# Kernel tuning notes

Measured on AMD Instinct MI355X. Metric: run time of the kernel, lower is better.

## Reference

```python
import jax, jax.numpy as jnp
import numpy as np

N = 100000   # nodes
E = 1600000  # edges
G = 512      # graphs in batch
F_IN = 128
H = 128
F_OUT = 1


def setup_inputs() -> dict:
    key = jax.random.key(0)
    ks = jax.random.split(key, 12)
    x = jax.random.normal(ks[0], (N, F_IN), dtype=jnp.float32)
    src = jax.random.randint(ks[1], (E,), 0, N, dtype=jnp.int32)
    dst = jax.random.randint(ks[2], (E,), 0, N, dtype=jnp.int32)
    node2graph = jnp.sort(jax.random.randint(ks[3], (N,), 0, G, dtype=jnp.int32))
    s_in = 1.0 / np.sqrt(F_IN)
    s_h = 1.0 / np.sqrt(H)
    W0 = jax.random.normal(ks[4], (F_IN, H), dtype=jnp.float32) * s_in
    b0 = jnp.zeros((H,), dtype=jnp.float32)
    W1 = jax.random.normal(ks[5], (H, H), dtype=jnp.float32) * s_h
    b1 = jnp.zeros((H,), dtype=jnp.float32)
    W2 = jax.random.normal(ks[6], (H, H), dtype=jnp.float32) * s_h
    b2 = jnp.zeros((H,), dtype=jnp.float32)
    Wm1 = jax.random.normal(ks[7], (H, H), dtype=jnp.float32) * s_h
    bm1 = jnp.zeros((H,), dtype=jnp.float32)
    Wm2 = jax.random.normal(ks[8], (H, F_OUT), dtype=jnp.float32) * s_h
    bm2 = jnp.zeros((F_OUT,), dtype=jnp.float32)
    return {"x": x, "src": src, "dst": dst, "node2graph": node2graph,
            "W0": W0, "b0": b0, "W1": W1, "b1": b1, "W2": W2, "b2": b2,
            "Wm1": Wm1, "bm1": bm1, "Wm2": Wm2, "bm2": bm2}


def _degree_norms(src, dst):
    ones = jnp.ones((E,), dtype=jnp.float32)
    out_deg = jax.ops.segment_sum(ones, src, num_segments=N)
    in_deg = jax.ops.segment_sum(ones, dst, num_segments=N)
    norm_out = jax.lax.rsqrt(jnp.maximum(out_deg, 1.0))  # [N]
    norm_in = jax.lax.rsqrt(jnp.maximum(in_deg, 1.0))    # [N]
    return norm_out, norm_in


def _graph_conv(x, src, dst, norm_out, norm_in, W, b):
    # DGL GraphConv, norm='both', in_feats <= out_feats path:
    # aggregate normalized src features, then linear + activation.
    xs = x * norm_out[:, None]
    msg = xs[src]                                         # [E, H] gather
    agg = jax.ops.segment_sum(msg, dst, num_segments=N)   # [N, H] scatter-add
    agg = agg * norm_in[:, None]
    return jax.nn.relu(agg @ W + b)


def reference(x, src, dst, node2graph, W0, b0, W1, b1, W2, b2, Wm1, bm1, Wm2, bm2):
    norm_out, norm_in = _degree_norms(src, dst)
    h = _graph_conv(x, src, dst, norm_out, norm_in, W0, b0)
    h = _graph_conv(h, src, dst, norm_out, norm_in, W1, b1)
    h = _graph_conv(h, src, dst, norm_out, norm_in, W2, b2)
    # sum_nodes readout per graph
    g = jax.ops.segment_sum(h, node2graph, num_segments=G)  # [G, H]
    # MLP head: Linear -> ReLU -> Linear
    return jax.nn.relu(g @ Wm1 + bm1) @ Wm2 + bm2           # [G, 1]
```

## Files before the change

### kernel.cpp

```cpp
#include <hip/hip_runtime.h>

#define NN 100000
#define NE 1600000
#define NG 512
#define HD 128

#define NBK 196
#define CHUNK 5120
#define NC 313
#define LH (2 * NBK * NC)

typedef _Float16 h8 __attribute__((ext_vector_type(8)));
typedef float f32x4 __attribute__((ext_vector_type(4)));

__global__ __launch_bounds__(1024) void k_hist(const int* __restrict__ src,
                                               const int* __restrict__ dst,
                                               int* __restrict__ H,
                                               const float* __restrict__ W0,
                                               const float* __restrict__ W1,
                                               const float* __restrict__ W2,
                                               _Float16* __restrict__ Bt) {
    if (blockIdx.x >= NC) {
        int i = (blockIdx.x - NC) * 1024 + threadIdx.x;
        int w = i >> 14;
        int rem = i & 16383;
        int n = rem >> 7;
        int k = rem & 127;
        const float* W = (w == 0) ? W0 : ((w == 1) ? W1 : W2);
        Bt[i] = (_Float16)W[k * 128 + n];
        return;
    }
    __shared__ int hd[NBK], hs[NBK];
    int c = blockIdx.x;
    for (int i = threadIdx.x; i < NBK; i += 1024) { hd[i] = 0; hs[i] = 0; }
    __syncthreads();
    int e0 = c * CHUNK;
    int e1 = e0 + CHUNK; if (e1 > NE) e1 = NE;
    for (int e = e0 + threadIdx.x; e < e1; e += 1024) {
        atomicAdd(&hd[dst[e] >> 9], 1);
        atomicAdd(&hs[src[e] >> 9], 1);
    }
    __syncthreads();
    for (int i = threadIdx.x; i < NBK; i += 1024) {
        H[i * NC + c] = hd[i];
        H[NBK * NC + i * NC + c] = hs[i];
    }
}

__global__ __launch_bounds__(256) void k_scan1g(int* __restrict__ H,
                                                int* __restrict__ bsum, int L) {
    __shared__ int s[256];
    int i = blockIdx.x * 256 + threadIdx.x;
    int v = (i < L) ? H[i] : 0;
    s[threadIdx.x] = v;
    __syncthreads();
    for (int off = 1; off < 256; off <<= 1) {
        int t = (threadIdx.x >= off) ? s[threadIdx.x - off] : 0;
        __syncthreads();
        s[threadIdx.x] += t;
        __syncthreads();
    }
    if (i < L) H[i] = s[threadIdx.x] - v;
    if (threadIdx.x == 255) bsum[blockIdx.x] = s[255];
}

__global__ __launch_bounds__(256) void k_scan3g(int* __restrict__ H,
                                                const int* __restrict__ bsum,
                                                int L, int nb) {
    __shared__ int sb[512];
    __shared__ int tmp2[256];
    int t = threadIdx.x;
    int b0 = (2 * t < nb) ? bsum[2 * t] : 0;
    int b1 = (2 * t + 1 < nb) ? bsum[2 * t + 1] : 0;
    int pair = b0 + b1;
    tmp2[t] = pair;
    __syncthreads();
    for (int off = 1; off < 256; off <<= 1) {
        int v2 = (t >= off) ? tmp2[t - off] : 0;
        __syncthreads();
        tmp2[t] += v2;
        __syncthreads();
    }
    int ex = tmp2[t] - pair;
    sb[2 * t] = ex;
    sb[2 * t + 1] = ex + b0;
    __syncthreads();
    int i = blockIdx.x * 256 + t;
    if (i < L) H[i] += sb[i >> 8];
}

__global__ __launch_bounds__(1024) void k_scatter(const int* __restrict__ src,
                                                  const int* __restrict__ dst,
                                                  const int* __restrict__ H,
                                                  int* __restrict__ dpart,
                                                  unsigned short* __restrict__ spart) {
    __shared__ int cd[NBK], cs[NBK];
    int c = blockIdx.x;
    for (int i = threadIdx.x; i < NBK; i += 1024) {
        cd[i] = H[i * NC + c];
        cs[i] = H[NBK * NC + i * NC + c] - NE;
    }
    __syncthreads();
    int e0 = c * CHUNK;
    int e1 = e0 + CHUNK; if (e1 > NE) e1 = NE;
    for (int e = e0 + threadIdx.x; e < e1; e += 1024) {
        int s = src[e], d = dst[e];
        int pd = atomicAdd(&cd[d >> 9], 1);
        dpart[pd] = s | ((d & 511) << 17);
        int ps = atomicAdd(&cs[s >> 9], 1);
        spart[ps] = (unsigned short)(s & 511);
    }
}

__global__ __launch_bounds__(1024) void k_bucket(const int* __restrict__ dpart,
                                                 const unsigned short* __restrict__ spart,
                                                 const int* __restrict__ H,
                                                 int* __restrict__ offs,
                                                 int* __restrict__ csr,
                                                 float* __restrict__ ni,
                                                 float* __restrict__ no) {
    __shared__ int deg[512];
    __shared__ int cur[512];
    __shared__ int tmp[1024];
    int b = blockIdx.x;
    bool isDst = (b < NBK);
    int bb = isDst ? b : b - NBK;
    int start, end;
    if (isDst) {
        start = H[bb * NC];
        end = (bb + 1 < NBK) ? H[(bb + 1) * NC] : NE;
    } else {
        start = H[NBK * NC + bb * NC] - NE;
        end = (bb + 1 < NBK) ? H[NBK * NC + (bb + 1) * NC] - NE : NE;
    }
    int t = threadIdx.x;
    if (t < 512) deg[t] = 0;
    __syncthreads();
    if (isDst) {
        for (int i = start + t; i < end; i += 1024)
            atomicAdd(&deg[(dpart[i] >> 17) & 511], 1);
    } else {
        for (int i = start + t; i < end; i += 1024)
            atomicAdd(&deg[spart[i]], 1);
    }
    __syncthreads();
    int vb = bb * 512;
    if (!isDst) {
        if (t < 512) {
            int v = vb + t;
            if (v < NN) no[v] = rsqrtf(fmaxf((float)deg[t], 1.0f));
        }
        return;
    }
    int a = (t < 512) ? deg[t] : 0;
    tmp[t] = a;
    __syncthreads();
    for (int off = 1; off < 1024; off <<= 1) {
        int v2 = (t >= off) ? tmp[t - off] : 0;
        __syncthreads();
        tmp[t] += v2;
        __syncthreads();
    }
    if (t < 512) {
        cur[t] = start + tmp[t] - a;
        int v = vb + t;
        if (v < NN) {
            offs[v] = cur[t];
            ni[v] = rsqrtf(fmaxf((float)a, 1.0f));
        }
    }
    if (b == NBK - 1 && t == 0) offs[NN] = NE;
    __syncthreads();
    for (int i = start + t; i < end; i += 1024) {
        int pk = dpart[i];
        int p = atomicAdd(&cur[(pk >> 17) & 511], 1);
        csr[p] = pk & 0x1FFFF;
    }
}

template <typename TA>
__global__ __launch_bounds__(256) void k_gemm_mfma(const TA* __restrict__ A,
                                                   const _Float16* __restrict__ Bt,
                                                   const float* __restrict__ no,
                                                   _Float16* __restrict__ Zh,
                                                   int nrows) {
    __shared__ _Float16 Bs[128 * 136];
    int tid = threadIdx.x;
    {
        const h8* B8 = (const h8*)Bt;
        h8* Bs8 = (h8*)Bs;
        for (int i = tid; i < 2048; i += 256) {
            int n = i >> 4, c = i & 15;
            Bs8[n * 17 + c] = B8[i];
        }
    }

    int wave = tid >> 6;
    int lane = tid & 63;
    int m16 = lane & 15;
    int quad = lane >> 4;
    int rowbase = blockIdx.x * 64 + wave * 16;
    int row = rowbase + m16;
    bool valid = row < nrows;

    h8 afrag[4];
    if (valid) {
        if constexpr (sizeof(TA) == 2) {
            const h8* Arow = (const h8*)(A + (size_t)row * 128);
#pragma unroll
            for (int kk = 0; kk < 4; kk++) afrag[kk] = Arow[kk * 4 + quad];
        } else {
            const float4* Arow = (const float4*)(A + (size_t)row * 128);
#pragma unroll
            for (int kk = 0; kk < 4; kk++) {
                float4 lo = Arow[kk * 8 + quad * 2];
                float4 hi = Arow[kk * 8 + quad * 2 + 1];
                h8 a;
                a[0] = (_Float16)lo.x; a[1] = (_Float16)lo.y;
                a[2] = (_Float16)lo.z; a[3] = (_Float16)lo.w;
                a[4] = (_Float16)hi.x; a[5] = (_Float16)hi.y;
                a[6] = (_Float16)hi.z; a[7] = (_Float16)hi.w;
                afrag[kk] = a;
            }
        }
    } else {
#pragma unroll
        for (int kk = 0; kk < 4; kk++) {
            h8 a;
#pragma unroll
            for (int j = 0; j < 8; j++) a[j] = (_Float16)0.f;
            afrag[kk] = a;
        }
    }

    __syncthreads();

    f32x4 acc[8];
#pragma unroll
    for (int nt = 0; nt < 8; nt++) acc[nt] = (f32x4){0.f, 0.f, 0.f, 0.f};

    const h8* Bs8 = (const h8*)Bs;
#pragma unroll
    for (int nt = 0; nt < 8; nt++) {
        const h8* Bp = Bs8 + (size_t)(nt * 16 + m16) * 17;
#pragma unroll
        for (int kk = 0; kk < 4; kk++) {
            acc[nt] = __builtin_amdgcn_mfma_f32_16x16x32_f16(afrag[kk], Bp[kk * 4 + quad],
                                                             acc[nt], 0, 0, 0);
        }
    }

    float nor[4];
#pragma unroll
    for (int r = 0; r < 4; r++) {
        int grow = rowbase + quad * 4 + r;
        nor[r] = (grow < nrows) ? no[grow] : 0.f;
    }

    __syncthreads();
    {
        int lr0 = wave * 16 + quad * 4;
#pragma unroll
        for (int nt = 0; nt < 8; nt++) {
#pragma unroll
            for (int r = 0; r < 4; r++) {
                Bs[(size_t)(lr0 + r) * 136 + nt * 16 + m16] =
                    (_Float16)(acc[nt][r] * nor[r]);
            }
        }
    }
    __syncthreads();

    int blockrow0 = blockIdx.x * 64;
    for (int i = tid; i < 1024; i += 256) {
        int r = i >> 4, cch = i & 15;
        int grow = blockrow0 + r;
        if (grow < nrows) {
            h8 val = *(const h8*)&Bs[(size_t)r * 136 + cch * 8];
            *(h8*)&Zh[(size_t)grow * 128 + cch * 8] = val;
        }
    }
}

__global__ __launch_bounds__(256) void k_agg(const h8* __restrict__ Zh,
                                             const int* __restrict__ offs,
                                             const int* __restrict__ csr,
                                             const float* __restrict__ ni,
                                             const float* __restrict__ b,
                                             h8* __restrict__ H16) {
    int v = blockIdx.x * 16 + (threadIdx.x >> 4);
    int c = threadIdx.x & 15;
    int s = offs[v];
    int e = offs[v + 1];
    float a0[8], a1[8];
#pragma unroll
    for (int j = 0; j < 8; j++) { a0[j] = 0.f; a1[j] = 0.f; }
    int i = s;
    for (; i + 4 <= e; i += 4) {
        int u0 = csr[i];
        int u1 = csr[i + 1];
        int u2 = csr[i + 2];
        int u3 = csr[i + 3];
        h8 z0 = Zh[(size_t)u0 * 16 + c];
        h8 z1 = Zh[(size_t)u1 * 16 + c];
        h8 z2 = Zh[(size_t)u2 * 16 + c];
        h8 z3 = Zh[(size_t)u3 * 16 + c];
#pragma unroll
        for (int j = 0; j < 8; j++) {
            a0[j] += (float)z0[j] + (float)z1[j];
            a1[j] += (float)z2[j] + (float)z3[j];
        }
    }
    for (; i < e; i++) {
        int u = csr[i];
        h8 z = Zh[(size_t)u * 16 + c];
#pragma unroll
        for (int j = 0; j < 8; j++) a0[j] += (float)z[j];
    }
    float niv = ni[v];
    const float* bb = b + c * 8;
    h8 r;
#pragma unroll
    for (int j = 0; j < 8; j++)
        r[j] = (_Float16)fmaxf((a0[j] + a1[j]) * niv + bb[j], 0.f);
    H16[(size_t)v * 16 + c] = r;
}

__global__ __launch_bounds__(256) void k_gsum(const h8* __restrict__ H8,
                                              const int* __restrict__ n2g,
                                              float* __restrict__ gbuf) {
    __shared__ float red[256 * 8];
    int gi = blockIdx.x >> 2;
    int part = blockIdx.x & 3;
    int t = threadIdx.x;
    int slot = t >> 4;
    int c = t & 15;

    int lo = 0, hi = NN;
    while (lo < hi) { int mid = (lo + hi) >> 1; if (n2g[mid] < gi) lo = mid + 1; else hi = mid; }
    int s = lo;
    hi = NN;
    while (lo < hi) { int mid = (lo + hi) >> 1; if (n2g[mid] < gi + 1) lo = mid + 1; else hi = mid; }
    int e = lo;

    float acc[8];
#pragma unroll
    for (int j = 0; j < 8; j++) acc[j] = 0.f;
    for (int v = s + part * 16 + slot; v < e; v += 64) {
        h8 z = H8[(size_t)v * 16 + c];
#pragma unroll
        for (int j = 0; j < 8; j++) acc[j] += (float)z[j];
    }
#pragma unroll
    for (int j = 0; j < 8; j++) red[t * 8 + j] = acc[j];
    __syncthreads();
    for (int off = 8; off >= 1; off >>= 1) {
        if (slot < off) {
#pragma unroll
            for (int j = 0; j < 8; j++)
                red[t * 8 + j] += red[(t + off * 16) * 8 + j];
        }
        __syncthreads();
    }
    if (slot == 0) {
#pragma unroll
        for (int j = 0; j < 8; j++)
            gbuf[((size_t)part * NG + gi) * 128 + c * 8 + j] = red[t * 8 + j];
    }
}

__global__ __launch_bounds__(128) void k_head(const float* __restrict__ gbuf,
                                              const float* __restrict__ Wm1,
                                              const float* __restrict__ bm1,
                                              const float* __restrict__ Wm2,
                                              const float* __restrict__ bm2,
                                              float* __restrict__ out) {
    __shared__ float gs[128];
    __shared__ float red2[128];
    int gi = blockIdx.x;
    int t = threadIdx.x;
    gs[t] = gbuf[(size_t)gi * 128 + t] +
            gbuf[((size_t)NG + gi) * 128 + t] +
            gbuf[((size_t)2 * NG + gi) * 128 + t] +
            gbuf[((size_t)3 * NG + gi) * 128 + t];
    __syncthreads();
    float a = bm1[t];
    for (int k = 0; k < 128; k++) a += gs[k] * Wm1[k * 128 + t];
    red2[t] = fmaxf(a, 0.f) * Wm2[t];
    __syncthreads();
    for (int s2 = 64; s2 > 0; s2 >>= 1) {
        if (t < s2) red2[t] += red2[t + s2];
        __syncthreads();
    }
    if (t == 0) out[gi] = red2[0] + bm2[0];
}

extern "C" void kernel_launch(void* const* d_in, const int* in_sizes, int n_in,
                              void* d_out, int out_size, void* d_ws, size_t ws_size,
                              hipStream_t stream) {
    const float* x   = (const float*)d_in[0];
    const int*   src = (const int*)d_in[1];
    const int*   dst = (const int*)d_in[2];
    const int*   n2g = (const int*)d_in[3];
    const float* W0  = (const float*)d_in[4];
    const float* b0  = (const float*)d_in[5];
    const float* W1  = (const float*)d_in[6];
    const float* b1  = (const float*)d_in[7];
    const float* W2  = (const float*)d_in[8];
    const float* b2  = (const float*)d_in[9];
    const float* Wm1 = (const float*)d_in[10];
    const float* bm1 = (const float*)d_in[11];
    const float* Wm2 = (const float*)d_in[12];
    const float* bm2 = (const float*)d_in[13];
    float* out = (float*)d_out;

    char* p = (char*)d_ws;
    auto carve = [&](size_t bytes) -> char* {
        char* r = p;
        p += (bytes + 255) & ~(size_t)255;
        return r;
    };
    _Float16* zh  = (_Float16*)carve((size_t)NN * HD * 2);
    _Float16* h16 = (_Float16*)carve((size_t)NN * HD * 2);
    _Float16* Bt  = (_Float16*)carve((size_t)3 * 128 * 128 * 2);
    float* no     = (float*)carve((size_t)NN * 4);
    float* ni     = (float*)carve((size_t)NN * 4);
    int*   offs   = (int*)carve((size_t)(NN + 1) * 4);
    int*   csr    = (int*)carve((size_t)NE * 4);
    int*   Hh     = (int*)carve((size_t)LH * 4);
    int*   bsum   = (int*)carve((size_t)512 * 4);
    int*   dpart  = (int*)carve((size_t)NE * 4);
    unsigned short* spart = (unsigned short*)carve((size_t)NE * 2);
    float* gbuf   = (float*)carve((size_t)4 * NG * 128 * 4);

    int scan_blocks = (LH + 255) / 256;
    k_hist<<<NC + 48, 1024, 0, stream>>>(src, dst, Hh, W0, W1, W2, Bt);
    k_scan1g<<<scan_blocks, 256, 0, stream>>>(Hh, bsum, LH);
    k_scan3g<<<scan_blocks, 256, 0, stream>>>(Hh, bsum, LH, scan_blocks);
    k_scatter<<<NC, 1024, 0, stream>>>(src, dst, Hh, dpart, spart);
    k_bucket<<<2 * NBK, 1024, 0, stream>>>(dpart, spart, Hh, offs, csr, ni, no);

    int gemm_blocks = (NN + 63) / 64;
    int agg_blocks  = NN / 16;

    k_gemm_mfma<float><<<gemm_blocks, 256, 0, stream>>>(x, Bt, no, zh, NN);
    k_agg<<<agg_blocks, 256, 0, stream>>>((const h8*)zh, offs, csr, ni, b0, (h8*)h16);
    k_gemm_mfma<_Float16><<<gemm_blocks, 256, 0, stream>>>(h16, Bt + 16384, no, zh, NN);
    k_agg<<<agg_blocks, 256, 0, stream>>>((const h8*)zh, offs, csr, ni, b1, (h8*)h16);
    k_gemm_mfma<_Float16><<<gemm_blocks, 256, 0, stream>>>(h16, Bt + 32768, no, zh, NN);
    k_agg<<<agg_blocks, 256, 0, stream>>>((const h8*)zh, offs, csr, ni, b2, (h8*)h16);

    k_gsum<<<NG * 4, 256, 0, stream>>>((const h8*)h16, n2g, gbuf);
    k_head<<<NG, 128, 0, stream>>>(gbuf, Wm1, bm1, Wm2, bm2, out);
}
```

Baseline: 387.0 us.

## Replace per-chunk histogram scan with global bucket totals and atomic cursor allocation

The edge partitioning no longer keeps a per-chunk histogram with a two-pass global scan. It now accumulates global bucket totals with atomics, scans only 392 entries in a single block, and has each scatter block reserve its output ranges with atomics on a global cursor. This drops one scan kernel and the large histogram buffer, and the chunk size is halved. In exchange, each scatter block recounts its edges, and the order of edges within a bucket becomes nondeterministic, which can change float summation order downstream.

```diff
diff --git a/kernel.cpp b/kernel.cpp
--- a/kernel.cpp
+++ b/kernel.cpp
@@ -6,22 +6,22 @@
 #define HD 128
 
 #define NBK 196
-#define CHUNK 5120
-#define NC 313
-#define LH (2 * NBK * NC)
+#define NB2 392
+#define CHUNK2 2560
+#define NC2 625
 
 typedef _Float16 h8 __attribute__((ext_vector_type(8)));
 typedef float f32x4 __attribute__((ext_vector_type(4)));
 
-__global__ __launch_bounds__(1024) void k_hist(const int* __restrict__ src,
-                                               const int* __restrict__ dst,
-                                               int* __restrict__ H,
-                                               const float* __restrict__ W0,
-                                               const float* __restrict__ W1,
-                                               const float* __restrict__ W2,
-                                               _Float16* __restrict__ Bt) {
-    if (blockIdx.x >= NC) {
-        int i = (blockIdx.x - NC) * 1024 + threadIdx.x;
+__global__ __launch_bounds__(1024) void k_count(const int* __restrict__ src,
+                                                const int* __restrict__ dst,
+                                                int* __restrict__ Btot,
+                                                const float* __restrict__ W0,
+                                                const float* __restrict__ W1,
+                                                const float* __restrict__ W2,
+                                                _Float16* __restrict__ Bt) {
+    if (blockIdx.x >= NC2) {
+        int i = (blockIdx.x - NC2) * 1024 + threadIdx.x;
         int w = i >> 14;
         int rem = i & 16383;
         int n = rem >> 7;
@@ -30,91 +30,72 @@
         Bt[i] = (_Float16)W[k * 128 + n];
         return;
     }
-    __shared__ int hd[NBK], hs[NBK];
-    int c = blockIdx.x;
-    for (int i = threadIdx.x; i < NBK; i += 1024) { hd[i] = 0; hs[i] = 0; }
-    __syncthreads();
-    int e0 = c * CHUNK;
-    int e1 = e0 + CHUNK; if (e1 > NE) e1 = NE;
-    for (int e = e0 + threadIdx.x; e < e1; e += 1024) {
-        atomicAdd(&hd[dst[e] >> 9], 1);
-        atomicAdd(&hs[src[e] >> 9], 1);
-    }
-    __syncthreads();
-    for (int i = threadIdx.x; i < NBK; i += 1024) {
-        H[i * NC + c] = hd[i];
-        H[NBK * NC + i * NC + c] = hs[i];
-    }
-}
-
-__global__ __launch_bounds__(256) void k_scan1g(int* __restrict__ H,
-                                                int* __restrict__ bsum, int L) {
-    __shared__ int s[256];
-    int i = blockIdx.x * 256 + threadIdx.x;
-    int v = (i < L) ? H[i] : 0;
-    s[threadIdx.x] = v;
-    __syncthreads();
-    for (int off = 1; off < 256; off <<= 1) {
-        int t = (threadIdx.x >= off) ? s[threadIdx.x - off] : 0;
-        __syncthreads();
-        s[threadIdx.x] += t;
-        __syncthreads();
-    }
-    if (i < L) H[i] = s[threadIdx.x] - v;
-    if (threadIdx.x == 255) bsum[blockIdx.x] = s[255];
-}
-
-__global__ __launch_bounds__(256) void k_scan3g(int* __restrict__ H,
-                                                const int* __restrict__ bsum,
-                                                int L, int nb) {
-    __shared__ int sb[512];
-    __shared__ int tmp2[256];
-    int t = threadIdx.x;
-    int b0 = (2 * t < nb) ? bsum[2 * t] : 0;
-    int b1 = (2 * t + 1 < nb) ? bsum[2 * t + 1] : 0;
-    int pair = b0 + b1;
-    tmp2[t] = pair;
-    __syncthreads();
-    for (int off = 1; off < 256; off <<= 1) {
-        int v2 = (t >= off) ? tmp2[t - off] : 0;
-        __syncthreads();
-        tmp2[t] += v2;
-        __syncthreads();
-    }
-    int ex = tmp2[t] - pair;
-    sb[2 * t] = ex;
-    sb[2 * t + 1] = ex + b0;
-    __syncthreads();
-    int i = blockIdx.x * 256 + t;
-    if (i < L) H[i] += sb[i >> 8];
-}
-
-__global__ __launch_bounds__(1024) void k_scatter(const int* __restrict__ src,
-                                                  const int* __restrict__ dst,
-                                                  const int* __restrict__ H,
-                                                  int* __restrict__ dpart,
-                                                  unsigned short* __restrict__ spart) {
-    __shared__ int cd[NBK], cs[NBK];
-    int c = blockIdx.x;
-    for (int i = threadIdx.x; i < NBK; i += 1024) {
-        cd[i] = H[i * NC + c];
-        cs[i] = H[NBK * NC + i * NC + c] - NE;
-    }
-    __syncthreads();
-    int e0 = c * CHUNK;
-    int e1 = e0 + CHUNK; if (e1 > NE) e1 = NE;
-    for (int e = e0 + threadIdx.x; e < e1; e += 1024) {
+    __shared__ int cnt[NB2];
+    int t = threadIdx.x;
+    if (t < NB2) cnt[t] = 0;
+    __syncthreads();
+    int e0 = blockIdx.x * CHUNK2;
+    int e1 = e0 + CHUNK2; if (e1 > NE) e1 = NE;
+    for (int e = e0 + t; e < e1; e += 1024) {
+        atomicAdd(&cnt[dst[e] >> 9], 1);
+        atomicAdd(&cnt[NBK + (src[e] >> 9)], 1);
+    }
+    __syncthreads();
+    if (t < NB2 && cnt[t]) atomicAdd(&Btot[t], cnt[t]);
+}
+
+__global__ __launch_bounds__(512) void k_base(const int* __restrict__ Btot,
+                                              int* __restrict__ base,
+                                              int* __restrict__ gcur) {
+    __shared__ int tmp[512];
+    int t = threadIdx.x;
+    int v = (t < NB2) ? Btot[t] : 0;
+    tmp[t] = v;
+    __syncthreads();
+    for (int off = 1; off < 512; off <<= 1) {
+        int v2 = (t >= off) ? tmp[t - off] : 0;
+        __syncthreads();
+        tmp[t] += v2;
+        __syncthreads();
+    }
+    int ex = tmp[t] - v;
+    if (t < NB2) {
+        base[t] = ex;
+        gcur[t] = ex;
+    }
+    if (t == 511) base[NB2] = tmp[511];
+}
+
+__global__ __launch_bounds__(1024) void k_scatter2(const int* __restrict__ src,
+                                                   const int* __restrict__ dst,
+                                                   int* __restrict__ gcur,
+                                                   int* __restrict__ dpart,
+                                                   unsigned short* __restrict__ spart) {
+    __shared__ int cnt[NB2], cur[NB2];
+    int t = threadIdx.x;
+    if (t < NB2) cnt[t] = 0;
+    __syncthreads();
+    int e0 = blockIdx.x * CHUNK2;
+    int e1 = e0 + CHUNK2; if (e1 > NE) e1 = NE;
+    for (int e = e0 + t; e < e1; e += 1024) {
+        atomicAdd(&cnt[dst[e] >> 9], 1);
+        atomicAdd(&cnt[NBK + (src[e] >> 9)], 1);
+    }
+    __syncthreads();
+    if (t < NB2) cur[t] = atomicAdd(&gcur[t], cnt[t]);
+    __syncthreads();
+    for (int e = e0 + t; e < e1; e += 1024) {
         int s = src[e], d = dst[e];
-        int pd = atomicAdd(&cd[d >> 9], 1);
+        int pd = atomicAdd(&cur[d >> 9], 1);
         dpart[pd] = s | ((d & 511) << 17);
-        int ps = atomicAdd(&cs[s >> 9], 1);
-        spart[ps] = (unsigned short)(s & 511);
+        int ps = atomicAdd(&cur[NBK + (s >> 9)], 1);
+        spart[ps - NE] = (unsigned short)(s & 511);
     }
 }
 
 __global__ __launch_bounds__(1024) void k_bucket(const int* __restrict__ dpart,
                                                  const unsigned short* __restrict__ spart,
-                                                 const int* __restrict__ H,
+                                                 const int* __restrict__ base,
                                                  int* __restrict__ offs,
                                                  int* __restrict__ csr,
                                                  float* __restrict__ ni,
@@ -127,11 +108,11 @@
     int bb = isDst ? b : b - NBK;
     int start, end;
     if (isDst) {
-        start = H[bb * NC];
-        end = (bb + 1 < NBK) ? H[(bb + 1) * NC] : NE;
+        start = base[bb];
+        end = base[bb + 1];
     } else {
-        start = H[NBK * NC + bb * NC] - NE;
-        end = (bb + 1 < NBK) ? H[NBK * NC + (bb + 1) * NC] - NE : NE;
+        start = base[NBK + bb] - NE;
+        end = base[NBK + bb + 1] - NE;
     }
     int t = threadIdx.x;
     if (t < 512) deg[t] = 0;
@@ -427,18 +408,18 @@
     float* ni     = (float*)carve((size_t)NN * 4);
     int*   offs   = (int*)carve((size_t)(NN + 1) * 4);
     int*   csr    = (int*)carve((size_t)NE * 4);
-    int*   Hh     = (int*)carve((size_t)LH * 4);
-    int*   bsum   = (int*)carve((size_t)512 * 4);
     int*   dpart  = (int*)carve((size_t)NE * 4);
     unsigned short* spart = (unsigned short*)carve((size_t)NE * 2);
+    int*   Btot   = (int*)carve((size_t)NB2 * 4);
+    int*   base   = (int*)carve((size_t)(NB2 + 1) * 4);
+    int*   gcur   = (int*)carve((size_t)NB2 * 4);
     float* gbuf   = (float*)carve((size_t)4 * NG * 128 * 4);
 
-    int scan_blocks = (LH + 255) / 256;
-    k_hist<<<NC + 48, 1024, 0, stream>>>(src, dst, Hh, W0, W1, W2, Bt);
-    k_scan1g<<<scan_blocks, 256, 0, stream>>>(Hh, bsum, LH);
-    k_scan3g<<<scan_blocks, 256, 0, stream>>>(Hh, bsum, LH, scan_blocks);
-    k_scatter<<<NC, 1024, 0, stream>>>(src, dst, Hh, dpart, spart);
-    k_bucket<<<2 * NBK, 1024, 0, stream>>>(dpart, spart, Hh, offs, csr, ni, no);
+    hipMemsetAsync(Btot, 0, (size_t)NB2 * 4, stream);
+    k_count<<<NC2 + 48, 1024, 0, stream>>>(src, dst, Btot, W0, W1, W2, Bt);
+    k_base<<<1, 512, 0, stream>>>(Btot, base, gcur);
+    k_scatter2<<<NC2, 1024, 0, stream>>>(src, dst, gcur, dpart, spart);
+    k_bucket<<<NB2, 1024, 0, stream>>>(dpart, spart, base, offs, csr, ni, no);
 
     int gemm_blocks = (NN + 63) / 64;
     int agg_blocks  = NN / 16;
```

Measured after the change: 404.7 us. 4.6% more time.

## Stage partitioned scatter and CSR writes in shared memory for coalesced stores

Applied to the files above, without the earlier changes.

The edge-partition scatter kernel now counts each chunk's bucket occupancy locally, runs a prefix sum, and stages edges in LDS sorted by bucket. It then writes them out contiguously per bucket instead of issuing random global stores straight from per-bucket atomics. The CSR bucket kernel similarly builds each bucket's CSR segment in a shared buffer and copies it out linearly, falling back to direct global writes when the bucket exceeds capacity. This is meant to turn scattered global writes into mostly coalesced ones, at the cost of extra passes over src/dst, more LDS use (lower occupancy), and additional barriers.

```diff
diff --git a/kernel.cpp b/kernel.cpp
--- a/kernel.cpp
+++ b/kernel.cpp
@@ -9,6 +9,7 @@
 #define CHUNK 5120
 #define NC 313
 #define LH (2 * NBK * NC)
+#define BCAP 11264
 
 typedef _Float16 h8 __attribute__((ext_vector_type(8)));
 typedef float f32x4 __attribute__((ext_vector_type(4)));
@@ -94,22 +95,79 @@
                                                   const int* __restrict__ H,
                                                   int* __restrict__ dpart,
                                                   unsigned short* __restrict__ spart) {
-    __shared__ int cd[NBK], cs[NBK];
+    __shared__ int valbuf[CHUNK];
+    __shared__ unsigned short bidbuf[CHUNK];
+    __shared__ int lcur[NBK], delta[NBK];
+    __shared__ int tmp[256];
     int c = blockIdx.x;
-    for (int i = threadIdx.x; i < NBK; i += 1024) {
-        cd[i] = H[i * NC + c];
-        cs[i] = H[NBK * NC + i * NC + c] - NE;
-    }
-    __syncthreads();
+    int t = threadIdx.x;
     int e0 = c * CHUNK;
     int e1 = e0 + CHUNK; if (e1 > NE) e1 = NE;
-    for (int e = e0 + threadIdx.x; e < e1; e += 1024) {
+    int n = e1 - e0;
+
+    for (int i = t; i < NBK; i += 1024) lcur[i] = 0;
+    __syncthreads();
+    for (int e = e0 + t; e < e1; e += 1024) atomicAdd(&lcur[dst[e] >> 9], 1);
+    __syncthreads();
+    {
+        int v = (t < NBK) ? lcur[t] : 0;
+        if (t < 256) tmp[t] = v;
+        __syncthreads();
+        for (int off = 1; off < 256; off <<= 1) {
+            int add = (t < 256 && t >= off) ? tmp[t - off] : 0;
+            __syncthreads();
+            if (t < 256) tmp[t] += add;
+            __syncthreads();
+        }
+        if (t < NBK) {
+            int lbase = tmp[t] - v;
+            lcur[t] = lbase;
+            delta[t] = H[t * NC + c] - lbase;
+        }
+    }
+    __syncthreads();
+    for (int e = e0 + t; e < e1; e += 1024) {
         int s = src[e], d = dst[e];
-        int pd = atomicAdd(&cd[d >> 9], 1);
-        dpart[pd] = s | ((d & 511) << 17);
-        int ps = atomicAdd(&cs[s >> 9], 1);
-        spart[ps] = (unsigned short)(s & 511);
-    }
+        int b = d >> 9;
+        int q = atomicAdd(&lcur[b], 1);
+        valbuf[q] = s | ((d & 511) << 17);
+        bidbuf[q] = (unsigned short)b;
+    }
+    __syncthreads();
+    for (int i = t; i < n; i += 1024) dpart[delta[bidbuf[i]] + i] = valbuf[i];
+    __syncthreads();
+
+    for (int i = t; i < NBK; i += 1024) lcur[i] = 0;
+    __syncthreads();
+    for (int e = e0 + t; e < e1; e += 1024) atomicAdd(&lcur[src[e] >> 9], 1);
+    __syncthreads();
+    {
+        int v = (t < NBK) ? lcur[t] : 0;
+        if (t < 256) tmp[t] = v;
+        __syncthreads();
+        for (int off = 1; off < 256; off <<= 1) {
+            int add = (t < 256 && t >= off) ? tmp[t - off] : 0;
+            __syncthreads();
+            if (t < 256) tmp[t] += add;
+            __syncthreads();
+        }
+        if (t < NBK) {
+            int lbase = tmp[t] - v;
+            lcur[t] = lbase;
+            delta[t] = H[NBK * NC + t * NC + c] - NE - lbase;
+        }
+    }
+    __syncthreads();
+    for (int e = e0 + t; e < e1; e += 1024) {
+        int s = src[e];
+        int b = s >> 9;
+        int q = atomicAdd(&lcur[b], 1);
+        valbuf[q] = s & 511;
+        bidbuf[q] = (unsigned short)b;
+    }
+    __syncthreads();
+    for (int i = t; i < n; i += 1024)
+        spart[delta[bidbuf[i]] + i] = (unsigned short)valbuf[i];
 }
 
 __global__ __launch_bounds__(1024) void k_bucket(const int* __restrict__ dpart,
@@ -120,8 +178,9 @@
                                                  float* __restrict__ ni,
                                                  float* __restrict__ no) {
     __shared__ int deg[512];
-    __shared__ int cur[512];
+    __shared__ int lcur[512];
     __shared__ int tmp[1024];
+    __shared__ int csrbuf[BCAP];
     int b = blockIdx.x;
     bool isDst = (b < NBK);
     int bb = isDst ? b : b - NBK;
@@ -162,19 +221,26 @@
         __syncthreads();
     }
     if (t < 512) {
-        cur[t] = start + tmp[t] - a;
+        lcur[t] = tmp[t] - a;
         int v = vb + t;
         if (v < NN) {
-            offs[v] = cur[t];
+            offs[v] = start + lcur[t];
             ni[v] = rsqrtf(fmaxf((float)a, 1.0f));
         }
     }
     if (b == NBK - 1 && t == 0) offs[NN] = NE;
     __syncthreads();
+    int len = end - start;
+    bool fits = (len <= BCAP);
     for (int i = start + t; i < end; i += 1024) {
         int pk = dpart[i];
-        int p = atomicAdd(&cur[(pk >> 17) & 511], 1);
-        csr[p] = pk & 0x1FFFF;
+        int q = atomicAdd(&lcur[(pk >> 17) & 511], 1);
+        if (fits) csrbuf[q] = pk & 0x1FFFF;
+        else      csr[start + q] = pk & 0x1FFFF;
+    }
+    __syncthreads();
+    if (fits) {
+        for (int i = t; i < len; i += 1024) csr[start + i] = csrbuf[i];
     }
 }
 
```

Measured after the change: 371.1 us. 4.1% less time.
